# Kernel optimization log

Hardware: AMD Instinct MI355X
Metric: run time of the kernel (lower is better)

Reference implementation:

```python
import jax, jax.numpy as jnp
import numpy as np

D_MODEL = 1024
D_STATE = 16
D_CONV = 4
EXPAND = 2
D_INNER = D_MODEL * EXPAND
DT_RANK = max(D_MODEL // 16, 1)  # 64
B, L = 2, 2048


def setup_inputs() -> dict:
    key = jax.random.key(0)
    ks = jax.random.split(key, 10)
    s = lambda fan_in: 1.0 / np.sqrt(fan_in)
    x = jax.random.normal(ks[0], (B, L, D_MODEL), dtype=jnp.float32)
    ln_w = jnp.ones((D_MODEL,), jnp.float32)
    ln_b = jnp.zeros((D_MODEL,), jnp.float32)
    in_proj_w = jax.random.normal(ks[1], (D_MODEL, 2 * D_INNER), jnp.float32) * s(D_MODEL)
    conv_w = jax.random.normal(ks[2], (D_INNER, D_CONV), jnp.float32) * s(D_CONV)
    conv_b = jnp.zeros((D_INNER,), jnp.float32)
    x_proj_w = jax.random.normal(ks[3], (D_INNER, DT_RANK + 2 * D_STATE), jnp.float32) * s(D_INNER)
    dt_proj_w = jax.random.normal(ks[4], (DT_RANK, D_INNER), jnp.float32) * s(DT_RANK)
    dt_proj_b = jax.random.normal(ks[5], (D_INNER,), jnp.float32) * 0.1
    # A_log init: log(arange(1, d_state+1)) broadcast over d_inner
    A_log = jnp.broadcast_to(jnp.log(jnp.arange(1, D_STATE + 1, dtype=jnp.float32))[None, :], (D_INNER, D_STATE)).copy()
    D_param = jnp.ones((D_INNER,), jnp.float32)
    out_proj_w = jax.random.normal(ks[6], (D_INNER, D_MODEL), jnp.float32) * s(D_INNER)
    res_scale = jnp.ones((1,), jnp.float32)
    return dict(x=x, ln_w=ln_w, ln_b=ln_b, in_proj_w=in_proj_w, conv_w=conv_w,
                conv_b=conv_b, x_proj_w=x_proj_w, dt_proj_w=dt_proj_w,
                dt_proj_b=dt_proj_b, A_log=A_log, D_param=D_param,
                out_proj_w=out_proj_w, res_scale=res_scale)


def _layernorm(x, w, b, eps=1e-5):
    mu = jnp.mean(x, axis=-1, keepdims=True)
    var = jnp.mean(jnp.square(x - mu), axis=-1, keepdims=True)
    return (x - mu) * jax.lax.rsqrt(var + eps) * w + b


def _causal_depthwise_conv1d(x_cl, conv_w, conv_b):
    # x_cl: [B, C, L]; conv_w: [C, K] depthwise; causal left-pad K-1
    out = jax.lax.conv_general_dilated(
        x_cl, conv_w[:, None, :],  # kernel [C,1,K]
        window_strides=(1,), padding=[(D_CONV - 1, 0)],
        dimension_numbers=('NCH', 'OIH', 'NCH'),
        feature_group_count=D_INNER)
    return out + conv_b[None, :, None]


def reference(x, ln_w, ln_b, in_proj_w, conv_w, conv_b, x_proj_w, dt_proj_w,
              dt_proj_b, A_log, D_param, out_proj_w, res_scale):
    residual = x
    xn = _layernorm(x, ln_w, ln_b)                       # [B,L,D]
    xz = xn @ in_proj_w                                  # [B,L,2*Di]
    x_main, z = jnp.split(xz, 2, axis=-1)                # each [B,L,Di]
    x_conv = _causal_depthwise_conv1d(jnp.swapaxes(x_main, 1, 2), conv_w, conv_b)
    new_conv_state = jnp.swapaxes(x_main, 1, 2)[:, :, -(D_CONV - 1):]
    x_main = jax.nn.silu(jnp.swapaxes(x_conv, 1, 2))     # [B,L,Di]

    A = -jnp.exp(A_log)                                  # [Di,N]
    x_dbl = x_main @ x_proj_w                            # [B,L,dt_rank+2N]
    dt, B_ssm, C_ssm = jnp.split(x_dbl, [DT_RANK, DT_RANK + D_STATE], axis=-1)
    dt = jax.nn.softplus(dt @ dt_proj_w + dt_proj_b)     # [B,L,Di]
    dA = jnp.exp(A[None, None] * dt[..., None])          # [B,L,Di,N]
    dBx = dt[..., None] * B_ssm[:, :, None, :] * x_main[..., None]  # [B,L,Di,N]

    def scan_fn(h, inp):
        dA_t, dBx_t, C_t = inp                           # [B,Di,N],[B,Di,N],[B,N]
        h = dA_t * h + dBx_t
        y_t = jnp.einsum('bdn,bn->bd', h, C_t)
        return h, y_t

    h0 = jnp.zeros((x.shape[0], D_INNER, D_STATE), x.dtype)
    new_ssm_state, ys = jax.lax.scan(
        scan_fn, h0,
        (jnp.swapaxes(dA, 0, 1), jnp.swapaxes(dBx, 0, 1), jnp.swapaxes(C_ssm, 0, 1)))
    y = jnp.swapaxes(ys, 0, 1)                           # [B,L,Di]
    y = y + x_main * D_param[None, None, :]
    y = y * jax.nn.silu(z)
    out = res_scale * (y @ out_proj_w) + residual        # [B,L,D]
    return out, new_ssm_state, new_conv_state
```

## Files before the change

### kernel.cpp

```cpp
#include <hip/hip_runtime.h>
#include <math.h>

#define D_MODEL 1024
#define D_STATE 16
#define D_CONVK 4
#define D_INNER 2048
#define DT_RANK 64
#define BB 2
#define LL 2048
#define NROWS (BB*LL)
#define NC 128
#define CH (LL/NC)
#define XZLD 4096
#define LOG2E 1.44269504088896340736f
#define LN2   0.69314718055994530942f

typedef __attribute__((ext_vector_type(8))) short bf16x8;
typedef __attribute__((ext_vector_type(8))) unsigned short u16x8;
typedef __attribute__((ext_vector_type(4))) float f32x4;

typedef __attribute__((address_space(3))) unsigned char lds_ucp;
typedef const __attribute__((address_space(1))) unsigned char glb_ucp;
#define GLD16(gp, lp) __builtin_amdgcn_global_load_lds((glb_ucp*)(gp), (lds_ucp*)(lp), 16, 0, 0)

__device__ inline unsigned short f2bf(float f) {
    union { float f; unsigned u; } c; c.f = f;
    unsigned r = c.u + 0x7fff + ((c.u >> 16) & 1);
    return (unsigned short)(r >> 16);
}
__device__ inline float bf2f(unsigned short s) {
    union { unsigned u; float f; } c; c.u = ((unsigned)s) << 16;
    return c.f;
}
__device__ inline float fexp2(float x) { return __builtin_amdgcn_exp2f(x); }
__device__ inline float frcp(float x)  { return __builtin_amdgcn_rcpf(x); }
__device__ inline float fsilu(float x) { return x * frcp(1.0f + fexp2(-x * LOG2E)); }

__global__ __launch_bounds__(256)
void prologue_kernel(const float* __restrict__ x, const float* __restrict__ lw,
                     const float* __restrict__ lb, unsigned short* __restrict__ xnb,
                     const float* __restrict__ Win, const float* __restrict__ Wout,
                     const float* __restrict__ Wx, const float* __restrict__ Wdt,
                     unsigned short* __restrict__ wtin, unsigned short* __restrict__ wtout,
                     unsigned short* __restrict__ Wxt, unsigned short* __restrict__ Wdtt) {
    if (blockIdx.x < NROWS) {
        int row = blockIdx.x;
        const float* xr = x + (size_t)row * D_MODEL;
        float4 v = ((const float4*)xr)[threadIdx.x];
        float s  = v.x + v.y + v.z + v.w;
        float ss = v.x*v.x + v.y*v.y + v.z*v.z + v.w*v.w;
        for (int off = 32; off > 0; off >>= 1) {
            s  += __shfl_down(s, off);
            ss += __shfl_down(ss, off);
        }
        __shared__ float red[8];
        int lane = threadIdx.x & 63, wv = threadIdx.x >> 6;
        if (lane == 0) { red[wv] = s; red[wv + 4] = ss; }
        __syncthreads();
        if (threadIdx.x == 0) {
            float ts  = red[0] + red[1] + red[2] + red[3];
            float tss = red[4] + red[5] + red[6] + red[7];
            float mu  = ts / D_MODEL;
            float var = tss / D_MODEL - mu * mu;
            red[0] = mu; red[1] = rsqrtf(var + 1e-5f);
        }
        __syncthreads();
        float mu = red[0], rs = red[1];
        float4 w4 = ((const float4*)lw)[threadIdx.x];
        float4 b4 = ((const float4*)lb)[threadIdx.x];
        ushort4 o;
        o.x = f2bf((v.x - mu) * rs * w4.x + b4.x);
        o.y = f2bf((v.y - mu) * rs * w4.y + b4.y);
        o.z = f2bf((v.z - mu) * rs * w4.z + b4.z);
        o.w = f2bf((v.w - mu) * rs * w4.w + b4.w);
        ((ushort4*)(xnb + (size_t)row * D_MODEL))[threadIdx.x] = o;
        return;
    }
    int tb = blockIdx.x - NROWS;
    int bx = tb % 228, by = tb / 228;
    __shared__ float t[32][33];
    const float* W; unsigned short* Wt; int K, Nsrc, xb;
    if (bx < 128)      { W = Win;  Wt = wtin;  K = 1024; Nsrc = 4096; xb = bx; }
    else if (bx < 160) { W = Wout; Wt = wtout; K = 2048; Nsrc = 1024; xb = bx - 128; }
    else if (bx < 164) { W = Wx;   Wt = Wxt;   K = 2048; Nsrc = 96;   xb = bx - 160; }
    else               { W = Wdt;  Wt = Wdtt;  K = 64;   Nsrc = 2048; xb = bx - 164; }
    int k0 = by * 32, n0 = xb * 32;
    if (k0 >= K) return;
    int tx = threadIdx.x & 31, ty = threadIdx.x >> 5;
#pragma unroll
    for (int i = 0; i < 32; i += 8)
        t[ty + i][tx] = (n0 + tx < Nsrc)
            ? W[(size_t)(k0 + ty + i) * Nsrc + n0 + tx] : 0.0f;
    __syncthreads();
#pragma unroll
    for (int i = 0; i < 32; i += 8)
        Wt[(size_t)(n0 + ty + i) * K + k0 + tx] = f2bf(t[tx][ty + i]);
}

__global__ __launch_bounds__(512, 2)
void mfma_gemm_pipe(const unsigned short* __restrict__ A,
                    const unsigned short* __restrict__ Wt,
                    int ldc, int K, unsigned short* __restrict__ out2) {
    __shared__ short As[4][256 * 32];
    __shared__ short Bs[4][256 * 32];
    int tid = threadIdx.x;
    int lane = tid & 63, w = tid >> 6;
    int wm = w & 1, wn = w >> 1;
    int bid = blockIdx.y * gridDim.x + blockIdx.x;
    int cpx = (gridDim.x * gridDim.y) >> 3;
    int swz = (bid & 7) * cpx + (bid >> 3);
    int bx = swz % gridDim.x, by = swz / gridDim.x;
    int row0 = by * 256, col0 = bx * 256;
    const unsigned short* gA0 = A  + (size_t)row0 * K;
    const unsigned short* gB0 = Wt + (size_t)col0 * K;
    int rowin = lane >> 2;
    int e8    = (((lane & 3) ^ (rowin & 3)) * 8);
    int quad = lane >> 4, r16 = lane & 15;
    int cslot = (quad ^ (r16 & 3)) * 8;
    f32x4 acc[8][4] = {};
    int nt = K >> 5;

#define STAGE_TILE(tt) do {                                                    \
    int _b = (tt) & 3; int _k0 = (tt) << 5;                                    \
    _Pragma("unroll")                                                          \
    for (int _r = 0; _r < 2; ++_r) {                                           \
        int _p = _r * 8 + w;                                                   \
        int _grow = _p * 16 + rowin;                                           \
        GLD16(gA0 + (size_t)_grow * K + _k0 + e8, (char*)&As[_b][0] + _p * 1024); \
        GLD16(gB0 + (size_t)_grow * K + _k0 + e8, (char*)&Bs[_b][0] + _p * 1024); \
    } } while (0)

    STAGE_TILE(0); STAGE_TILE(1); STAGE_TILE(2);
    for (int t = 0; t < nt; ++t) {
        if (t < nt - 2)       asm volatile("s_waitcnt vmcnt(8)" ::: "memory");
        else if (t == nt - 2) asm volatile("s_waitcnt vmcnt(4)" ::: "memory");
        else                  asm volatile("s_waitcnt vmcnt(0)" ::: "memory");
        __builtin_amdgcn_s_barrier();
        __builtin_amdgcn_sched_barrier(0);
        if (t + 3 < nt) STAGE_TILE(t + 3);
        const short* Ab = &As[t & 3][0];
        const short* Bb = &Bs[t & 3][0];
        bf16x8 bfr[4], af[8];
#pragma unroll
        for (int i = 0; i < 4; ++i)
            bfr[i] = *(const bf16x8*)&Bb[(wn * 64 + i * 16 + r16) * 32 + cslot];
#pragma unroll
        for (int i = 0; i < 8; ++i)
            af[i] = *(const bf16x8*)&Ab[(wm * 128 + i * 16 + r16) * 32 + cslot];
        __builtin_amdgcn_s_setprio(1);
#pragma unroll
        for (int mi = 0; mi < 8; ++mi)
#pragma unroll
            for (int ni = 0; ni < 4; ++ni)
                acc[mi][ni] = __builtin_amdgcn_mfma_f32_16x16x32_bf16(
                    af[mi], bfr[ni], acc[mi][ni], 0, 0, 0);
        __builtin_amdgcn_s_setprio(0);
    }
#undef STAGE_TILE
    int odd = lane & 1;
#pragma unroll
    for (int mi = 0; mi < 8; ++mi)
#pragma unroll
        for (int ni = 0; ni < 4; ++ni) {
            int colE = col0 + wn * 64 + ni * 16 + r16;
#pragma unroll
            for (int rp = 0; rp < 2; ++rp) {
                int rowE = row0 + wm * 128 + mi * 16 + quad * 4 + rp * 2;
                int row  = rowE + odd;
                int colp = colE - odd;
                unsigned hh = (unsigned)f2bf(acc[mi][ni][rp*2]) |
                              ((unsigned)f2bf(acc[mi][ni][rp*2+1]) << 16);
                unsigned ph = __shfl_xor((int)hh, 1);
                unsigned u_even = (hh & 0xffffu) | (ph << 16);
                unsigned u_odd  = (ph >> 16) | (hh & 0xffff0000u);
                unsigned u = odd ? u_odd : u_even;
                *(unsigned*)&out2[(size_t)row * ldc + colp] = u;
            }
        }
}

__global__ __launch_bounds__(256)
void mfma_gemm(const unsigned short* __restrict__ A,
               const unsigned short* __restrict__ Wt,
               float* __restrict__ C, int ldc, int K, int kchunk,
               size_t zstride, int mode,
               const float* __restrict__ aux,
               int Ncols, unsigned short* __restrict__ out2) {
    __shared__ short As[128 * 64];
    __shared__ short Bs[128 * 64];
    int tid = threadIdx.x;
    int lane = tid & 63, w = tid >> 6;
    int wm = w & 1, wn = w >> 1;
    int row0 = blockIdx.y * 128, col0 = blockIdx.x * 128;
    int kb = blockIdx.z * kchunk, ke = kb + kchunk;
    C += (size_t)blockIdx.z * zstride;
    f32x4 acc[4][4] = {};
    const unsigned short* gA0 = A  + (size_t)row0 * K;
    const unsigned short* gB0 = Wt + (size_t)col0 * K;
    int r_in = lane >> 3;
    int e16  = (lane & 7) * 8;
    int quad = lane >> 4, r16 = lane & 15;
    for (int k0 = kb; k0 < ke; k0 += 64) {
        __syncthreads();
#pragma unroll
        for (int t = 0; t < 4; ++t) {
            int p = w * 4 + t;
            int row = p * 8 + r_in;
            GLD16(gA0 + (size_t)row * K + k0 + e16, (char*)As + p * 1024);
            GLD16(gB0 + (size_t)row * K + k0 + e16, (char*)Bs + p * 1024);
        }
        __syncthreads();
#pragma unroll
        for (int ks = 0; ks < 2; ++ks) {
            bf16x8 af[4], bfr[4];
#pragma unroll
            for (int i = 0; i < 4; ++i) {
                af[i]  = *(const bf16x8*)&As[(wm * 64 + i * 16 + r16) * 64 + ks * 32 + quad * 8];
                bfr[i] = *(const bf16x8*)&Bs[(wn * 64 + i * 16 + r16) * 64 + ks * 32 + quad * 8];
            }
#pragma unroll
            for (int mi = 0; mi < 4; ++mi)
#pragma unroll
                for (int ni = 0; ni < 4; ++ni)
                    acc[mi][ni] = __builtin_amdgcn_mfma_f32_16x16x32_bf16(
                        af[mi], bfr[ni], acc[mi][ni], 0, 0, 0);
        }
    }
    int odd = lane & 1;
#pragma unroll
    for (int mi = 0; mi < 4; ++mi)
#pragma unroll
        for (int ni = 0; ni < 4; ++ni) {
            int colE = col0 + wn * 64 + ni * 16 + r16;
            float v[4];
#pragma unroll
            for (int r = 0; r < 4; ++r) v[r] = acc[mi][ni][r];
            if (mode == 4) {
                float bv = aux[colE];
#pragma unroll
                for (int r = 0; r < 4; ++r) {
                    float tv = v[r] + bv;
                    v[r] = (tv > 20.0f) ? tv
                         : LN2 * __builtin_amdgcn_logf(1.0f + fexp2(tv * LOG2E));
                }
            }
#pragma unroll
            for (int rp = 0; rp < 2; ++rp) {
                int rowE = row0 + wm * 64 + mi * 16 + quad * 4 + rp * 2;
                int row  = rowE + odd;
                int colp = colE - odd;
                if (mode >= 3) {
                    unsigned hh = (unsigned)f2bf(v[rp*2]) | ((unsigned)f2bf(v[rp*2+1]) << 16);
                    unsigned ph = __shfl_xor((int)hh, 1);
                    unsigned u_even = (hh & 0xffffu) | (ph << 16);
                    unsigned u_odd  = (ph >> 16) | (hh & 0xffff0000u);
                    unsigned u = odd ? u_odd : u_even;
                    *(unsigned*)&out2[(size_t)row * ldc + colp] = u;
                } else {
                    float a0 = v[rp*2], a1 = v[rp*2+1];
                    float b0 = __shfl_xor(a0, 1), b1 = __shfl_xor(a1, 1);
                    float2 f2;
                    f2.x = odd ? b1 : a0;
                    f2.y = odd ? a1 : b0;
                    if (colp < Ncols)
                        *(float2*)&C[(size_t)row * ldc + colp] = f2;
                }
            }
        }
}

__global__ __launch_bounds__(256)
void xdbl_reduce(const float* __restrict__ P,
                 unsigned short* __restrict__ xdtr, float* __restrict__ xbc) {
    const int S1 = NROWS * 96;
    int t = blockIdx.x * 256 + threadIdx.x;
    float s = 0.0f;
#pragma unroll
    for (int k = 0; k < 8; ++k) s += P[t + k * S1];
    int row = t / 96, col = t - row * 96;
    if (col < DT_RANK) xdtr[(size_t)row * DT_RANK + col] = f2bf(s);
    else xbc[(size_t)row * 32 + col - DT_RANK] = s;
}

__global__ __launch_bounds__(256)
void out_final(const float* __restrict__ P0, const float* __restrict__ P1,
               const float* __restrict__ x, const float* __restrict__ rscale,
               float* __restrict__ out) {
    int t = blockIdx.x * 256 + threadIdx.x;
    float rs = rscale[0];
    float4 a = ((const float4*)P0)[t];
    float4 b = ((const float4*)P1)[t];
    float4 r = ((const float4*)x)[t];
    float4 o;
    o.x = rs * (a.x + b.x) + r.x;
    o.y = rs * (a.y + b.y) + r.y;
    o.z = rs * (a.z + b.z) + r.z;
    o.w = rs * (a.w + b.w) + r.w;
    ((float4*)out)[t] = o;
}

__global__ __launch_bounds__(256)
void conv_kernel(const unsigned short* __restrict__ xzb, const float* __restrict__ cw,
                 const float* __restrict__ cb, unsigned short* __restrict__ xs,
                 float* __restrict__ conv_state_out) {
    int loct = blockIdx.x & 255;
    int b    = blockIdx.x >> 8;
    int d0   = threadIdx.x * 8;
    float wgt[8][4];
#pragma unroll
    for (int j = 0; j < 8; ++j) {
        float4 w4 = *(const float4*)(cw + (size_t)(d0 + j) * 4);
        wgt[j][0] = w4.x; wgt[j][1] = w4.y; wgt[j][2] = w4.z; wgt[j][3] = w4.w;
    }
    float bias[8];
    *(float4*)&bias[0] = *(const float4*)(cb + d0);
    *(float4*)&bias[4] = *(const float4*)(cb + d0 + 4);
    float xr[11][8];
#pragma unroll
    for (int r = 0; r < 11; ++r) {
        int l = loct * 8 - 3 + r;
        if (l >= 0) {
            u16x8 v = *(const u16x8*)&xzb[((size_t)b * LL + l) * XZLD + d0];
#pragma unroll
            for (int j = 0; j < 8; ++j) xr[r][j] = bf2f(v[j]);
        } else {
#pragma unroll
            for (int j = 0; j < 8; ++j) xr[r][j] = 0.0f;
        }
    }
#pragma unroll
    for (int i = 0; i < 8; ++i) {
        unsigned short o[8];
#pragma unroll
        for (int j = 0; j < 8; ++j) {
            float a = bias[j];
#pragma unroll
            for (int k = 0; k < 4; ++k) a = fmaf(xr[i + k][j], wgt[j][k], a);
            o[j] = f2bf(fsilu(a));
        }
        *(u16x8*)&xs[((size_t)b * LL + loct * 8 + i) * D_INNER + d0] = *(u16x8*)o;
    }
    if (loct == 255) {
#pragma unroll
        for (int i = 8; i < 11; ++i)
#pragma unroll
            for (int j = 0; j < 8; ++j)
                conv_state_out[((size_t)b * D_INNER + d0 + j) * 3 + (i - 8)] = xr[i][j];
    }
}

__global__ __launch_bounds__(256)
void scan_part1(const unsigned short* __restrict__ dt, const float* __restrict__ xbc,
                const unsigned short* __restrict__ xs,
                const float* __restrict__ A_log,
                float* __restrict__ Sbuf, float* __restrict__ Tbuf) {
    __shared__ float Bs[CH][32];
    int d = blockIdx.x * 256 + threadIdx.x;
    int c = blockIdx.y, b = blockIdx.z;
    size_t rowbase = (size_t)b * LL + (size_t)c * CH;
    for (int e = threadIdx.x; e < CH * 32; e += 256) {
        int i = e >> 5, j = e & 31;
        Bs[i][j] = xbc[(rowbase + i) * 32 + j];
    }
    float al2[16];
    {
        const float4* ap = (const float4*)(A_log + (size_t)d * D_STATE);
#pragma unroll
        for (int q = 0; q < 4; ++q) {
            float4 a4 = ap[q];
            al2[q*4+0] = -fexp2(a4.x * LOG2E) * LOG2E;
            al2[q*4+1] = -fexp2(a4.y * LOG2E) * LOG2E;
            al2[q*4+2] = -fexp2(a4.z * LOG2E) * LOG2E;
            al2[q*4+3] = -fexp2(a4.w * LOG2E) * LOG2E;
        }
    }
    __syncthreads();
    float S[16];
#pragma unroll
    for (int n = 0; n < 16; ++n) S[n] = 0.0f;
    float Tsum = 0.0f;
    float dtv = bf2f(dt[rowbase * D_INNER + d]);
    float xv  = bf2f(xs[rowbase * D_INNER + d]);
    for (int i = 0; i < CH; ++i) {
        float dtn = 0.0f, xn2 = 0.0f;
        if (i + 1 < CH) {
            size_t r2 = (rowbase + i + 1) * D_INNER + d;
            dtn = bf2f(dt[r2]); xn2 = bf2f(xs[r2]);
        }
        Tsum += dtv;
        float dtx = dtv * xv;
#pragma unroll
        for (int q = 0; q < 4; ++q) {
            float4 Bv = *(const float4*)&Bs[i][q * 4];
            S[q*4+0] = fmaf(fexp2(al2[q*4+0] * dtv), S[q*4+0], dtx * Bv.x);
            S[q*4+1] = fmaf(fexp2(al2[q*4+1] * dtv), S[q*4+1], dtx * Bv.y);
            S[q*4+2] = fmaf(fexp2(al2[q*4+2] * dtv), S[q*4+2], dtx * Bv.z);
            S[q*4+3] = fmaf(fexp2(al2[q*4+3] * dtv), S[q*4+3], dtx * Bv.w);
        }
        dtv = dtn; xv = xn2;
    }
    size_t o = (((size_t)b * NC + c) * D_INNER + d) * D_STATE;
#pragma unroll
    for (int q = 0; q < 4; ++q) {
        float4 Sv;
        Sv.x = S[q*4+0]; Sv.y = S[q*4+1]; Sv.z = S[q*4+2]; Sv.w = S[q*4+3];
        *(float4*)(Sbuf + o + q * 4) = Sv;
    }
    Tbuf[((size_t)b * NC + c) * D_INNER + d] = Tsum;
}

__global__ __launch_bounds__(256)
void scan_part2(const float* __restrict__ S, const float* __restrict__ Tbuf,
                const float* __restrict__ A_log, float* __restrict__ Hin) {
    int t = blockIdx.x * 256 + threadIdx.x;
    int b = t >> 15;
    int rem = t & 32767;
    int d = rem >> 4;
    float al2 = -fexp2(A_log[rem] * LOG2E) * LOG2E;
    size_t sbase = (size_t)b * NC * (D_INNER * D_STATE) + rem;
    size_t tbase = (size_t)b * NC * D_INNER + d;
    float h = 0.0f;
    for (int c = 0; c < NC; ++c) {
        size_t sq = sbase + (size_t)c * (D_INNER * D_STATE);
        float s = S[sq];
        float T = Tbuf[tbase + (size_t)c * D_INNER];
        Hin[sq] = h;
        h = fmaf(fexp2(al2 * T), h, s);
    }
}

__global__ __launch_bounds__(256)
void scan_part3(const unsigned short* __restrict__ dt, const float* __restrict__ xbc,
                const unsigned short* __restrict__ xs,
                const unsigned short* __restrict__ xzb,
                const float* __restrict__ A_log, const float* __restrict__ Dp,
                const float* __restrict__ Hin,
                unsigned short* __restrict__ y, float* __restrict__ ssm_out) {
    __shared__ float Bs[CH][32];
    int d = blockIdx.x * 256 + threadIdx.x;
    int c = blockIdx.y, b = blockIdx.z;
    size_t rowbase = (size_t)b * LL + (size_t)c * CH;
    for (int e = threadIdx.x; e < CH * 32; e += 256) {
        int i = e >> 5, j = e & 31;
        Bs[i][j] = xbc[(rowbase + i) * 32 + j];
    }
    float al2[16];
    {
        const float4* ap = (const float4*)(A_log + (size_t)d * D_STATE);
#pragma unroll
        for (int q = 0; q < 4; ++q) {
            float4 a4 = ap[q];
            al2[q*4+0] = -fexp2(a4.x * LOG2E) * LOG2E;
            al2[q*4+1] = -fexp2(a4.y * LOG2E) * LOG2E;
            al2[q*4+2] = -fexp2(a4.z * LOG2E) * LOG2E;
            al2[q*4+3] = -fexp2(a4.w * LOG2E) * LOG2E;
        }
    }
    float Dv = Dp[d];
    float h[16];
    {
        const float4* hp = (const float4*)(Hin + (((size_t)b * NC + c) * D_INNER + d) * D_STATE);
#pragma unroll
        for (int q = 0; q < 4; ++q) {
            float4 h4 = hp[q];
            h[q*4+0] = h4.x; h[q*4+1] = h4.y; h[q*4+2] = h4.z; h[q*4+3] = h4.w;
        }
    }
    __syncthreads();
    size_t r0 = rowbase * D_INNER + d;
    float dtv = bf2f(dt[r0]);
    float xv  = bf2f(xs[r0]);
    float zv  = bf2f(xzb[rowbase * XZLD + D_INNER + d]);
    for (int i = 0; i < CH; ++i) {
        float dtn = 0.0f, xn2 = 0.0f, zn2 = 0.0f;
        if (i + 1 < CH) {
            size_t r2 = (rowbase + i + 1) * D_INNER + d;
            dtn = bf2f(dt[r2]); xn2 = bf2f(xs[r2]);
            zn2 = bf2f(xzb[(rowbase + i + 1) * XZLD + D_INNER + d]);
        }
        float dtx = dtv * xv;
        float yv = 0.0f;
#pragma unroll
        for (int q = 0; q < 4; ++q) {
            float4 Bv = *(const float4*)&Bs[i][q * 4];
            float4 Cv = *(const float4*)&Bs[i][16 + q * 4];
            h[q*4+0] = fmaf(fexp2(al2[q*4+0] * dtv), h[q*4+0], dtx * Bv.x);
            h[q*4+1] = fmaf(fexp2(al2[q*4+1] * dtv), h[q*4+1], dtx * Bv.y);
            h[q*4+2] = fmaf(fexp2(al2[q*4+2] * dtv), h[q*4+2], dtx * Bv.z);
            h[q*4+3] = fmaf(fexp2(al2[q*4+3] * dtv), h[q*4+3], dtx * Bv.w);
            yv = fmaf(h[q*4+0], Cv.x, yv);
            yv = fmaf(h[q*4+1], Cv.y, yv);
            yv = fmaf(h[q*4+2], Cv.z, yv);
            yv = fmaf(h[q*4+3], Cv.w, yv);
        }
        yv = (yv + xv * Dv) * fsilu(zv);
        y[(rowbase + i) * D_INNER + d] = f2bf(yv);
        dtv = dtn; xv = xn2; zv = zn2;
    }
    if (c == NC - 1) {
        float* sp = ssm_out + ((size_t)b * D_INNER + d) * D_STATE;
#pragma unroll
        for (int q = 0; q < 4; ++q) {
            float4 h4;
            h4.x = h[q*4+0]; h4.y = h[q*4+1]; h4.z = h[q*4+2]; h4.w = h[q*4+3];
            *(float4*)(sp + q * 4) = h4;
        }
    }
}

extern "C" void kernel_launch(void* const* d_in, const int* in_sizes, int n_in,
                              void* d_out, int out_size, void* d_ws, size_t ws_size,
                              hipStream_t stream) {
    (void)in_sizes; (void)n_in; (void)out_size; (void)ws_size;
    const float* x      = (const float*)d_in[0];
    const float* ln_w   = (const float*)d_in[1];
    const float* ln_b   = (const float*)d_in[2];
    const float* Win    = (const float*)d_in[3];
    const float* convw  = (const float*)d_in[4];
    const float* convb  = (const float*)d_in[5];
    const float* Wx     = (const float*)d_in[6];
    const float* Wdt    = (const float*)d_in[7];
    const float* bdt    = (const float*)d_in[8];
    const float* A_log  = (const float*)d_in[9];
    const float* Dp     = (const float*)d_in[10];
    const float* Wout   = (const float*)d_in[11];
    const float* rscale = (const float*)d_in[12];

    float* out      = (float*)d_out;
    float* ssm_out  = out + (size_t)NROWS * D_MODEL;
    float* conv_out = ssm_out + (size_t)BB * D_INNER * D_STATE;

    float* ws = (float*)d_ws;
    unsigned short* xzb = (unsigned short*)ws;
    unsigned short* xsb = xzb + (size_t)NROWS * XZLD;
    unsigned short* dtbb = xsb + (size_t)NROWS * D_INNER;
    float* xbc  = (float*)(dtbb + (size_t)NROWS * D_INNER);
    unsigned short* xdtr = (unsigned short*)(xbc + (size_t)NROWS * 32);
    unsigned short* xnb  = xdtr + (size_t)NROWS * DT_RANK;
    unsigned short* wtin = xnb + (size_t)NROWS * D_MODEL;
    unsigned short* wtout = wtin + (size_t)(2 * D_INNER) * D_MODEL;
    unsigned short* Wxt  = wtout + (size_t)D_MODEL * D_INNER;
    unsigned short* Wdtt = Wxt + (size_t)128 * D_INNER;
    float* Tbuf = (float*)(Wdtt + (size_t)D_INNER * DT_RANK);
    float* Sbuf = Tbuf + (size_t)BB * NC * D_INNER;
    float* Pxdbl = Sbuf;
    float* Hin   = Sbuf;
    float* P0 = Sbuf;
    float* P1 = Sbuf + (size_t)NROWS * D_MODEL;
    unsigned short* ybuf = xnb;

    prologue_kernel<<<NROWS + 228 * 64, 256, 0, stream>>>(
        x, ln_w, ln_b, xnb, Win, Wout, Wx, Wdt, wtin, wtout, Wxt, Wdtt);

    mfma_gemm_pipe<<<dim3(2 * D_INNER / 256, NROWS / 256), 512, 0, stream>>>(
        xnb, wtin, XZLD, D_MODEL, xzb);

    conv_kernel<<<BB * (LL / 8), 256, 0, stream>>>(
        xzb, convw, convb, xsb, conv_out);

    mfma_gemm<<<dim3(1, NROWS / 128, 8), 256, 0, stream>>>(
        xsb, Wxt, Pxdbl, 96, D_INNER, D_INNER / 8, (size_t)NROWS * 96, 0,
        nullptr, 96, nullptr);
    xdbl_reduce<<<(NROWS * 96) / 256, 256, 0, stream>>>(Pxdbl, xdtr, xbc);

    mfma_gemm<<<dim3(D_INNER / 128, NROWS / 128), 256, 0, stream>>>(
        xdtr, Wdtt, nullptr, D_INNER, DT_RANK, DT_RANK, 0, 4,
        bdt, D_INNER, dtbb);

    scan_part1<<<dim3(D_INNER / 256, NC, BB), 256, 0, stream>>>(
        dtbb, xbc, xsb, A_log, Sbuf, Tbuf);
    scan_part2<<<(BB * D_INNER * D_STATE) / 256, 256, 0, stream>>>(
        Sbuf, Tbuf, A_log, Hin);
    scan_part3<<<dim3(D_INNER / 256, NC, BB), 256, 0, stream>>>(
        dtbb, xbc, xsb, xzb, A_log, Dp, Hin, ybuf, ssm_out);

    mfma_gemm<<<dim3(D_MODEL / 128, NROWS / 128, 2), 256, 0, stream>>>(
        ybuf, wtout, P0, D_MODEL, D_INNER, D_INNER / 2,
        (size_t)NROWS * D_MODEL, 0,
        nullptr, D_MODEL, nullptr);

    out_final<<<(NROWS * D_MODEL) / (256 * 4), 256, 0, stream>>>(
        P0, P1, x, rscale, out);
}
```

Baseline: 310.3 us.

## Restructure GEMM main loop into split A/B staging with ping-pong MFMA halves

Reworks the bf16 MFMA GEMM pipeline from a depth-3 prefetch with one barrier per tile into a depth-2 prefetch. A and B loads are staged separately and interleaved between two half-tile MFMA phases, with more barriers per iteration. The LDS swizzle also changes to a new XOR pattern, aiming to reduce bank conflicts and balance memory and matrix work. The extra barriers and shallower prefetch could expose more load latency.

```diff
diff --git a/kernel.cpp b/kernel.cpp
--- a/kernel.cpp
+++ b/kernel.cpp
@@ -114,49 +114,73 @@
     const unsigned short* gA0 = A  + (size_t)row0 * K;
     const unsigned short* gB0 = Wt + (size_t)col0 * K;
     int rowin = lane >> 2;
-    int e8    = (((lane & 3) ^ (rowin & 3)) * 8);
+    int scol  = ((lane & 3) ^ ((lane >> 3) & 3)) << 3;
     int quad = lane >> 4, r16 = lane & 15;
-    int cslot = (quad ^ (r16 & 3)) * 8;
+    int swr  = (r16 >> 1) & 3;
+    int cslot = ((quad ^ swr) << 3);
     f32x4 acc[8][4] = {};
     int nt = K >> 5;
 
-#define STAGE_TILE(tt) do {                                                    \
-    int _b = (tt) & 3; int _k0 = (tt) << 5;                                    \
+#define STAGE_A(tt) do { int _b = (tt) & 3; int _k0 = (tt) << 5;               \
     _Pragma("unroll")                                                          \
-    for (int _r = 0; _r < 2; ++_r) {                                           \
-        int _p = _r * 8 + w;                                                   \
-        int _grow = _p * 16 + rowin;                                           \
-        GLD16(gA0 + (size_t)_grow * K + _k0 + e8, (char*)&As[_b][0] + _p * 1024); \
-        GLD16(gB0 + (size_t)_grow * K + _k0 + e8, (char*)&Bs[_b][0] + _p * 1024); \
+    for (int _l = 0; _l < 2; ++_l) {                                           \
+        int _c = _l * 8 + w;                                                   \
+        GLD16(gA0 + (size_t)(_c * 16 + rowin) * K + _k0 + scol,                \
+              (char*)&As[_b][0] + _c * 1024);                                  \
     } } while (0)
-
-    STAGE_TILE(0); STAGE_TILE(1); STAGE_TILE(2);
+#define STAGE_B(tt) do { int _b = (tt) & 3; int _k0 = (tt) << 5;               \
+    _Pragma("unroll")                                                          \
+    for (int _l = 0; _l < 2; ++_l) {                                           \
+        int _c = _l * 8 + w;                                                   \
+        GLD16(gB0 + (size_t)(_c * 16 + rowin) * K + _k0 + scol,                \
+              (char*)&Bs[_b][0] + _c * 1024);                                  \
+    } } while (0)
+
+    STAGE_A(0); STAGE_B(0); STAGE_A(1); STAGE_B(1);
+    asm volatile("s_waitcnt vmcnt(4)" ::: "memory");
+    __builtin_amdgcn_s_barrier();
+
+#pragma unroll 4
     for (int t = 0; t < nt; ++t) {
-        if (t < nt - 2)       asm volatile("s_waitcnt vmcnt(8)" ::: "memory");
-        else if (t == nt - 2) asm volatile("s_waitcnt vmcnt(4)" ::: "memory");
-        else                  asm volatile("s_waitcnt vmcnt(0)" ::: "memory");
-        __builtin_amdgcn_s_barrier();
-        __builtin_amdgcn_sched_barrier(0);
-        if (t + 3 < nt) STAGE_TILE(t + 3);
         const short* Ab = &As[t & 3][0];
         const short* Bb = &Bs[t & 3][0];
-        bf16x8 bfr[4], af[8];
+        bf16x8 bfr[4], af[4];
 #pragma unroll
         for (int i = 0; i < 4; ++i)
             bfr[i] = *(const bf16x8*)&Bb[(wn * 64 + i * 16 + r16) * 32 + cslot];
 #pragma unroll
-        for (int i = 0; i < 8; ++i)
+        for (int i = 0; i < 4; ++i)
             af[i] = *(const bf16x8*)&Ab[(wm * 128 + i * 16 + r16) * 32 + cslot];
+        if (t + 2 < nt) STAGE_A(t + 2);
+        __builtin_amdgcn_s_barrier();
         __builtin_amdgcn_s_setprio(1);
 #pragma unroll
-        for (int mi = 0; mi < 8; ++mi)
+        for (int mi = 0; mi < 4; ++mi)
 #pragma unroll
             for (int ni = 0; ni < 4; ++ni)
                 acc[mi][ni] = __builtin_amdgcn_mfma_f32_16x16x32_bf16(
                     af[mi], bfr[ni], acc[mi][ni], 0, 0, 0);
         __builtin_amdgcn_s_setprio(0);
-    }
-#undef STAGE_TILE
+        __builtin_amdgcn_s_barrier();
+#pragma unroll
+        for (int i = 0; i < 4; ++i)
+            af[i] = *(const bf16x8*)&Ab[(wm * 128 + (4 + i) * 16 + r16) * 32 + cslot];
+        if (t + 2 < nt) STAGE_B(t + 2);
+        __builtin_amdgcn_s_barrier();
+        __builtin_amdgcn_s_setprio(1);
+#pragma unroll
+        for (int mi = 0; mi < 4; ++mi)
+#pragma unroll
+            for (int ni = 0; ni < 4; ++ni)
+                acc[4 + mi][ni] = __builtin_amdgcn_mfma_f32_16x16x32_bf16(
+                    af[mi], bfr[ni], acc[4 + mi][ni], 0, 0, 0);
+        __builtin_amdgcn_s_setprio(0);
+        if (t < nt - 2)       asm volatile("s_waitcnt vmcnt(4)" ::: "memory");
+        else if (t == nt - 2) asm volatile("s_waitcnt vmcnt(0)" ::: "memory");
+        __builtin_amdgcn_s_barrier();
+    }
+#undef STAGE_A
+#undef STAGE_B
     int odd = lane & 1;
 #pragma unroll
     for (int mi = 0; mi < 8; ++mi)
```

New measurement: 300.3 us. 1.03x faster.
